# Optimization experiments

Hardware: AMD Instinct MI355X
Metric: run time of the kernel (lower is better)

## Reference

```python
import jax, jax.numpy as jnp
import numpy as np
import math

DIM = 1024
NUM_HEADS = 16


def setup_inputs() -> dict:
    key = jax.random.key(0)
    ks = jax.random.split(key, 6)
    B, S, D = 2, 2048, DIM
    return {
        "q": jax.random.normal(ks[0], (B, S, D), dtype=jnp.float32),
        "k": jax.random.normal(ks[1], (B, S, D), dtype=jnp.float32),
        "v": jax.random.normal(ks[2], (B, S, D), dtype=jnp.float32),
        "wq": jax.random.normal(ks[3], (D, D), dtype=jnp.float32),
        "wk": jax.random.normal(ks[4], (D, D), dtype=jnp.float32),
        "wv": jax.random.normal(ks[5], (D, D), dtype=jnp.float32),
    }


def reference(q, k, v, wq, wk, wv):
    B, S, D = q.shape
    H = NUM_HEADS
    hd = D // H
    # projections: [B,S,D] @ [D,D]
    qp = (q @ wq).reshape(B, H, S, hd)  # NOTE: direct reshape, as in the original
    kp = (k @ wk).reshape(B, H, S, hd)
    vp = (v @ wv).reshape(B, H, S, hd)
    scale = 1.0 / math.sqrt(D)  # original scales by sqrt(dim), not sqrt(head_dim)
    att = jnp.einsum("bhqd,bhkd->bhqk", qp, kp) * scale  # [B,H,S,S]
    att = jax.nn.softmax(att, axis=-1)
    out = jnp.einsum("bhqk,bhkd->bhqd", att, vp)  # [B,H,S,hd]
    out = out.transpose(0, 2, 1, 3).reshape(B, S, D)
    return out
```

## Files before the change

### kernel.cpp

```cpp
#include <hip/hip_runtime.h>
#include <hip/hip_bf16.h>
#include <stdint.h>

#define DIMD 1024
#define SEQ  2048
#define NH   16
#define MROWS 4096
#define NQ   65536

typedef __bf16 bf16_t;
typedef bf16_t bf16x8 __attribute__((ext_vector_type(8)));
typedef float  f32x4  __attribute__((ext_vector_type(4)));
typedef unsigned short u16;
typedef unsigned short u16x4 __attribute__((ext_vector_type(4)));
typedef unsigned short u16x8 __attribute__((ext_vector_type(8)));
typedef unsigned int   u32;
typedef u32 u32x2 __attribute__((ext_vector_type(2)));

static __device__ __forceinline__ f32x4 mfma16(bf16x8 a, bf16x8 b, f32x4 c) {
    return __builtin_amdgcn_mfma_f32_16x16x32_bf16(a, b, c, 0, 0, 0);
}

static __device__ __forceinline__ float fast_exp2(float x) {
#if __has_builtin(__builtin_amdgcn_exp2f)
    return __builtin_amdgcn_exp2f(x);
#else
    return exp2f(x);
#endif
}

#define GLD16(gsrc, ldst) __builtin_amdgcn_global_load_lds(                    \
    (const __attribute__((address_space(1))) unsigned int*)(gsrc),             \
    (__attribute__((address_space(3))) unsigned int*)(ldst), 16, 0, 0)

static __device__ __forceinline__ void split_bf16(float x, u16& h, u16& l) {
    u32 u = __float_as_uint(x);
    u16 hu = (u16)(u >> 16);
    float xh = __uint_as_float((u32)hu << 16);
    float lo = x - xh;
    h = hu;
    l = (u16)(__float_as_uint(lo) >> 16);
}

static __device__ __forceinline__ u32 pack_bf16(float a, float b) {
    return (__float_as_uint(a) >> 16) | (__float_as_uint(b) & 0xffff0000u);
}
static __device__ __forceinline__ u32 pack_bf16_rn(float a, float b) {
    u32 ua = __float_as_uint(a) + 0x8000u;
    u32 ub = __float_as_uint(b) + 0x8000u;
    return (ua >> 16) | (ub & 0xffff0000u);
}
static __device__ __forceinline__ float bf_to_f(u16 v) {
    return __uint_as_float((u32)v << 16);
}

__global__ __launch_bounds__(256) void transWs3(
    const float* __restrict__ w0, const float* __restrict__ w1, const float* __restrict__ w2,
    u16* __restrict__ WTsH, u16* __restrict__ WTsL) {
    const int z = blockIdx.z;
    const float* W = z == 0 ? w0 : z == 1 ? w1 : w2;
    __shared__ u16 Hs[4096], Ls[4096];
    const int tid = threadIdx.x;
    const int kt = blockIdx.x, nt = blockIdx.y;
    const int n0 = nt * 128, k0 = kt * 32;
    #pragma unroll
    for (int i = 0; i < 4; i++) {
        int f = i * 256 + tid;
        int kr = f >> 5, nc4 = (f & 31) * 4;
        f32x4 w = *(const f32x4*)&W[(size_t)(k0 + kr) * DIMD + n0 + nc4];
        int cc = kr >> 3, e = kr & 7;
        #pragma unroll
        for (int j = 0; j < 4; j++) {
            u16 hh, ll; split_bf16(w[j], hh, ll);
            Hs[cc * 1024 + (nc4 + j) * 8 + e] = hh;
            Ls[cc * 1024 + (nc4 + j) * 8 + e] = ll;
        }
    }
    __syncthreads();
    const size_t base = (size_t)z * (DIMD * DIMD) + (size_t)(nt * 32 + kt) * 4096;
    #pragma unroll
    for (int i = 0; i < 2; i++) {
        int idx = (i * 256 + tid) * 8;
        *(u16x8*)(WTsH + base + idx) = *(const u16x8*)&Hs[idx];
        *(u16x8*)(WTsL + base + idx) = *(const u16x8*)&Ls[idx];
    }
}

__global__ __launch_bounds__(256, 3) void proj7(
    const float* __restrict__ xq, const float* __restrict__ xk, const float* __restrict__ xv,
    const u16* __restrict__ WTsH, const u16* __restrict__ WTsL,
    u16* __restrict__ qh, u16* __restrict__ ql,
    u16* __restrict__ kh, u16* __restrict__ kl,
    u16* __restrict__ vh) {

    const int z = blockIdx.z;
    const float* X = z == 0 ? xq : z == 1 ? xk : xv;
    const u16* BH = WTsH + (size_t)z * (DIMD * DIMD);
    const u16* BL = WTsL + (size_t)z * (DIMD * DIMD);
    u16* outH = z == 0 ? qh : z == 1 ? kh : vh;
    u16* outL = z == 0 ? ql : kl;
    const float oscale = z == 0 ? 0.0450842200278f : 1.0f;

    __shared__ u16 lds[24576];
    u16* AsH = lds;
    u16* AsL = lds + 4096;

    const int tid  = threadIdx.x;
    const int lane = tid & 63, wave = tid >> 6;
    const int quad = lane >> 4, l16 = lane & 15;
    const int wy = wave >> 1, wx = wave & 1;
    const int m0 = blockIdx.x * 128;
    const int n0 = blockIdx.y * 128;
    const size_t Bregion0 = (size_t)(blockIdx.y * 32) * 4096;

    const int rA  = tid >> 2, ccA = tid & 3;
    const int idxA0 = ccA * 1024 + ((rA ^ (ccA << 1)) * 8);
    const int idxA1 = idxA0 + 512;
    const float* Xb0 = X + (size_t)(m0 + rA) * DIMD + ccA * 8;
    const float* Xb1 = X + (size_t)(m0 + rA + 64) * DIMD + ccA * 8;

    f32x4 acc[4][4];
    #pragma unroll
    for (int mt = 0; mt < 4; mt++)
        #pragma unroll
        for (int nt = 0; nt < 4; nt++) acc[mt][nt] = (f32x4)0.0f;

    f32x4 pa0, pa1, pa2, pa3;

#define LOADA(kt) do {                                                         \
        pa0 = *(const f32x4*)(Xb0 + (kt) * 32);                                \
        pa1 = *(const f32x4*)(Xb0 + (kt) * 32 + 4);                            \
        pa2 = *(const f32x4*)(Xb1 + (kt) * 32);                                \
        pa3 = *(const f32x4*)(Xb1 + (kt) * 32 + 4);                            \
    } while (0)

#define WRITEA() do {                                                          \
        u16x8 h, l;                                                            \
        _Pragma("unroll")                                                      \
        for (int j = 0; j < 4; j++) {                                          \
            u16 hh, ll;                                                        \
            split_bf16(pa0[j], hh, ll); h[j] = hh;     l[j] = ll;              \
            split_bf16(pa1[j], hh, ll); h[4 + j] = hh; l[4 + j] = ll;          \
        }                                                                      \
        *(u16x8*)&AsH[idxA0] = h;                                              \
        *(u16x8*)&AsL[idxA0] = l;                                              \
        _Pragma("unroll")                                                      \
        for (int j = 0; j < 4; j++) {                                          \
            u16 hh, ll;                                                        \
            split_bf16(pa2[j], hh, ll); h[j] = hh;     l[j] = ll;              \
            split_bf16(pa3[j], hh, ll); h[4 + j] = hh; l[4 + j] = ll;          \
        }                                                                      \
        *(u16x8*)&AsH[idxA1] = h;                                              \
        *(u16x8*)&AsL[idxA1] = l;                                              \
    } while (0)

#define STAGEB(kt, buf) do {                                                   \
        const size_t rb = Bregion0 + (size_t)(kt) * 4096;                      \
        u16* BsHd = lds + 8192 + (buf) * 8192;                                 \
        u16* BsLd = BsHd + 4096;                                               \
        int c0 = tid, c1 = 256 + tid;                                          \
        GLD16(BH + rb + c0 * 8, &BsHd[c0 * 8]);                                \
        GLD16(BH + rb + c1 * 8, &BsHd[c1 * 8]);                                \
        GLD16(BL + rb + c0 * 8, &BsLd[c0 * 8]);                                \
        GLD16(BL + rb + c1 * 8, &BsLd[c1 * 8]);                                \
    } while (0)

    LOADA(0);
    STAGEB(0, 0);
    WRITEA();
    __syncthreads();

    for (int kt = 0; kt < 32; kt++) {
        const int cur = kt & 1;
        if (kt < 31) {
            LOADA(kt + 1);
            STAGEB(kt + 1, cur ^ 1);
        }

        const u16* BsH = lds + 8192 + cur * 8192;
        const u16* BsL = BsH + 4096;

        bf16x8 aH[4], aL[4], bH[4], bL[4];
        #pragma unroll
        for (int mt = 0; mt < 4; mt++) {
            int r = wy * 64 + mt * 16 + l16;
            int idx = quad * 1024 + ((r ^ (quad << 1)) * 8);
            aH[mt] = *(const bf16x8*)&AsH[idx];
            aL[mt] = *(const bf16x8*)&AsL[idx];
        }
        #pragma unroll
        for (int nt = 0; nt < 4; nt++) {
            int r = wx * 64 + nt * 16 + l16;
            bH[nt] = *(const bf16x8*)&BsH[(quad * 128 + r) * 8];
            bL[nt] = *(const bf16x8*)&BsL[(quad * 128 + r) * 8];
        }
        #pragma unroll
        for (int mt = 0; mt < 4; mt++)
            #pragma unroll
            for (int nt = 0; nt < 4; nt++) {
                acc[mt][nt] = mfma16(aH[mt], bH[nt], acc[mt][nt]);
                acc[mt][nt] = mfma16(aH[mt], bL[nt], acc[mt][nt]);
                acc[mt][nt] = mfma16(aL[mt], bH[nt], acc[mt][nt]);
            }

        __syncthreads();
        if (kt < 31) WRITEA();
        __syncthreads();
    }
#undef LOADA
#undef WRITEA
#undef STAGEB

    #pragma unroll
    for (int mt = 0; mt < 4; mt++)
        #pragma unroll
        for (int nt = 0; nt < 4; nt++)
            #pragma unroll
            for (int r = 0; r < 4; r++) {
                int row = m0 + wy * 64 + mt * 16 + quad * 4 + r;
                int col = n0 + wx * 64 + nt * 16 + l16;
                u16 hh, ll; split_bf16(acc[mt][nt][r] * oscale, hh, ll);
                outH[(size_t)row * DIMD + col] = hh;
                if (z != 2) outL[(size_t)row * DIMD + col] = ll;
            }
}

__global__ __launch_bounds__(256) void transposeV(
    const u16* __restrict__ vh, u16* __restrict__ vt) {
    __shared__ u16 Ls[64][72];
    const int tid = threadIdx.x;
    const int bh = blockIdx.y;
    const int s0 = blockIdx.x * 64;
    const size_t slab = (size_t)bh * (SEQ * 64);
    #pragma unroll
    for (int i = 0; i < 2; i++) {
        int f = i * 256 + tid;
        int r = f >> 3, c = (f & 7) * 8;
        *(u16x8*)&Ls[r][c] = *(const u16x8*)(vh + slab + (size_t)(s0 + r) * 64 + c);
    }
    __syncthreads();
    #pragma unroll
    for (int i = 0; i < 2; i++) {
        int f = i * 256 + tid;
        int d = f >> 3, j = (f & 7) * 8;
        u16x8 o;
        #pragma unroll
        for (int jj = 0; jj < 8; jj++) o[jj] = Ls[j + jj][d];
        *(u16x8*)(vt + slab + (size_t)d * SEQ + s0 + j) = o;
    }
}

__global__ __launch_bounds__(256, 2) void flash9(
    const u16* __restrict__ qh, const u16* __restrict__ ql,
    const u16* __restrict__ kh, const u16* __restrict__ kl,
    const u16* __restrict__ vt,
    u16* __restrict__ Opart, float* __restrict__ Mpart, float* __restrict__ Lpart) {

    __shared__ u16 KH[64][72], KL[64][72], VTs[64][72];
    __shared__ u16 Ps[4][16][72];

    const int tid  = threadIdx.x;
    const int lane = tid & 63, wv = tid >> 6;
    const int quad = lane >> 4, l16 = lane & 15;
    const int bh = blockIdx.x, z = blockIdx.z;
    const size_t slab = (size_t)bh * (SEQ * 64);
    const int q0 = blockIdx.y * 128 + wv * 32;
    const int jbase = z * 1024;

    bf16x8 qfH[2][2], qfL[2][2];
    #pragma unroll
    for (int mq = 0; mq < 2; mq++) {
        const size_t rb = slab + (size_t)(q0 + mq * 16 + l16) * 64;
        #pragma unroll
        for (int kk = 0; kk < 2; kk++) {
            qfH[mq][kk] = *(const bf16x8*)(qh + rb + kk * 32 + quad * 8);
            qfL[mq][kk] = *(const bf16x8*)(ql + rb + kk * 32 + quad * 8);
        }
    }

    f32x4 O[2][4];
    float M[2] = {-3.0e38f, -3.0e38f}, L[2] = {0.0f, 0.0f};
    #pragma unroll
    for (int mq = 0; mq < 2; mq++)
        #pragma unroll
        for (int nv = 0; nv < 4; nv++) O[mq][nv] = (f32x4)0.0f;

    const int f0 = tid, f1 = 256 + tid;
    const int r0 = f0 >> 3, c0 = (f0 & 7) * 8;
    const int r1 = f1 >> 3, c1 = (f1 & 7) * 8;
    u16x8 s0, s1, s2, s3, s4, s5;

    {
        const int j0 = jbase;
        s0 = *(const u16x8*)(kh + slab + (size_t)(j0 + r0) * 64 + c0);
        s1 = *(const u16x8*)(kh + slab + (size_t)(j0 + r1) * 64 + c1);
        s2 = *(const u16x8*)(kl + slab + (size_t)(j0 + r0) * 64 + c0);
        s3 = *(const u16x8*)(kl + slab + (size_t)(j0 + r1) * 64 + c1);
        s4 = *(const u16x8*)(vt + slab + (size_t)r0 * SEQ + j0 + c0);
        s5 = *(const u16x8*)(vt + slab + (size_t)r1 * SEQ + j0 + c1);
    }
    *(u16x8*)&KH[r0][c0] = s0;  *(u16x8*)&KH[r1][c1] = s1;
    *(u16x8*)&KL[r0][c0] = s2;  *(u16x8*)&KL[r1][c1] = s3;
    *(u16x8*)&VTs[r0][c0] = s4; *(u16x8*)&VTs[r1][c1] = s5;
    __syncthreads();

    for (int t = 0; t < 16; t++) {
        if (t < 15) {
            const int j0 = jbase + (t + 1) * 64;
            s0 = *(const u16x8*)(kh + slab + (size_t)(j0 + r0) * 64 + c0);
            s1 = *(const u16x8*)(kh + slab + (size_t)(j0 + r1) * 64 + c1);
            s2 = *(const u16x8*)(kl + slab + (size_t)(j0 + r0) * 64 + c0);
            s3 = *(const u16x8*)(kl + slab + (size_t)(j0 + r1) * 64 + c1);
            s4 = *(const u16x8*)(vt + slab + (size_t)r0 * SEQ + j0 + c0);
            s5 = *(const u16x8*)(vt + slab + (size_t)r1 * SEQ + j0 + c1);
        }

        f32x4 St[2][4];
        #pragma unroll
        for (int mq = 0; mq < 2; mq++)
            #pragma unroll
            for (int nt = 0; nt < 4; nt++) St[mq][nt] = (f32x4)0.0f;
        __builtin_amdgcn_s_setprio(1);
        #pragma unroll
        for (int nt = 0; nt < 4; nt++) {
            const int rB = nt * 16 + l16;
            #pragma unroll
            for (int kk = 0; kk < 2; kk++) {
                bf16x8 kHf = *(const bf16x8*)&KH[rB][kk * 32 + quad * 8];
                bf16x8 kLf = *(const bf16x8*)&KL[rB][kk * 32 + quad * 8];
                #pragma unroll
                for (int mq = 0; mq < 2; mq++) {
                    St[mq][nt] = mfma16(kHf, qfH[mq][kk], St[mq][nt]);
                    St[mq][nt] = mfma16(kLf, qfH[mq][kk], St[mq][nt]);
                    St[mq][nt] = mfma16(kHf, qfL[mq][kk], St[mq][nt]);
                }
            }
        }
        __builtin_amdgcn_s_setprio(0);

        #pragma unroll
        for (int mq = 0; mq < 2; mq++) {
            float mx = St[mq][0][0];
            #pragma unroll
            for (int nt = 0; nt < 4; nt++)
                #pragma unroll
                for (int r = 0; r < 4; r++) mx = fmaxf(mx, St[mq][nt][r]);
            mx = fmaxf(mx, __shfl_xor(mx, 16));
            mx = fmaxf(mx, __shfl_xor(mx, 32));
            float Mn = M[mq];
            if (__any(mx > Mn)) {
                Mn = fmaxf(Mn, mx);
                float al = fast_exp2(M[mq] - Mn);
                M[mq] = Mn;
                L[mq] *= al;
                #pragma unroll
                for (int nv = 0; nv < 4; nv++) O[mq][nv] *= al;
            }
            float rs = 0.0f;
            #pragma unroll
            for (int nt = 0; nt < 4; nt++)
                #pragma unroll
                for (int r = 0; r < 4; r++) {
                    float p = fast_exp2(St[mq][nt][r] - Mn);
                    St[mq][nt][r] = p;
                    rs += p;
                }
            rs += __shfl_xor(rs, 16);
            rs += __shfl_xor(rs, 32);
            L[mq] += rs;
            #pragma unroll
            for (int nt = 0; nt < 4; nt++) {
                u32x2 d;
                d[0] = pack_bf16(St[mq][nt][0], St[mq][nt][1]);
                d[1] = pack_bf16(St[mq][nt][2], St[mq][nt][3]);
                *(u32x2*)&Ps[wv][l16][nt * 16 + quad * 4] = d;
            }

            __builtin_amdgcn_s_setprio(1);
            #pragma unroll
            for (int kk = 0; kk < 2; kk++) {
                bf16x8 pB = *(const bf16x8*)&Ps[wv][l16][kk * 32 + quad * 8];
                #pragma unroll
                for (int nv = 0; nv < 4; nv++) {
                    bf16x8 vF = *(const bf16x8*)&VTs[nv * 16 + l16][kk * 32 + quad * 8];
                    O[mq][nv] = mfma16(vF, pB, O[mq][nv]);
                }
            }
            __builtin_amdgcn_s_setprio(0);
        }

        __syncthreads();
        if (t < 15) {
            *(u16x8*)&KH[r0][c0] = s0;  *(u16x8*)&KH[r1][c1] = s1;
            *(u16x8*)&KL[r0][c0] = s2;  *(u16x8*)&KL[r1][c1] = s3;
            *(u16x8*)&VTs[r0][c0] = s4; *(u16x8*)&VTs[r1][c1] = s5;
        }
        __syncthreads();
    }

    const int qgb = bh * SEQ + q0;
    #pragma unroll
    for (int mq = 0; mq < 2; mq++) {
        const int qg = qgb + mq * 16 + l16;
        #pragma unroll
        for (int nv = 0; nv < 4; nv++) {
            u32x2 d;
            d[0] = pack_bf16_rn(O[mq][nv][0], O[mq][nv][1]);
            d[1] = pack_bf16_rn(O[mq][nv][2], O[mq][nv][3]);
            *(u32x2*)(Opart + ((size_t)(z * NQ + qg)) * 64 + nv * 16 + quad * 4) = d;
        }
        if (quad == 0) {
            Mpart[z * NQ + qg] = M[mq];
            Lpart[z * NQ + qg] = L[mq];
        }
    }
}

__global__ __launch_bounds__(256) void combineK(
    const u16* __restrict__ Opart, const float* __restrict__ Mpart,
    const float* __restrict__ Lpart, float* __restrict__ out) {
    int idx = blockIdx.x * 256 + threadIdx.x;
    int qg = idx >> 4, c4 = (idx & 15) * 4;
    float M0 = Mpart[qg], M1 = Mpart[NQ + qg];
    float L0 = Lpart[qg], L1 = Lpart[NQ + qg];
    float Ms = fmaxf(M0, M1);
    float w0 = fast_exp2(M0 - Ms), w1 = fast_exp2(M1 - Ms);
    float inv = 1.0f / (w0 * L0 + w1 * L1);
    u16x4 a = *(const u16x4*)&Opart[(size_t)qg * 64 + c4];
    u16x4 b = *(const u16x4*)&Opart[((size_t)NQ + qg) * 64 + c4];
    f32x4 o;
    #pragma unroll
    for (int j = 0; j < 4; j++)
        o[j] = (w0 * bf_to_f(a[j]) + w1 * bf_to_f(b[j])) * inv;
    int bh = qg >> 11, s = qg & 2047;
    int bb = bh >> 4, h = bh & 15;
    *(f32x4*)&out[((size_t)(bb * SEQ + s)) * DIMD + h * 64 + c4] = o;
}

extern "C" void kernel_launch(void* const* d_in, const int* in_sizes, int n_in,
                              void* d_out, int out_size, void* d_ws, size_t ws_size,
                              hipStream_t stream) {
    const float* q  = (const float*)d_in[0];
    const float* k  = (const float*)d_in[1];
    const float* v  = (const float*)d_in[2];
    const float* wq = (const float*)d_in[3];
    const float* wk = (const float*)d_in[4];
    const float* wv = (const float*)d_in[5];
    float* out = (float*)d_out;

    char* ws = (char*)d_ws;
    const size_t MB = 1 << 20;
    u16* qh   = (u16*)(ws + 0 * MB);
    u16* ql   = (u16*)(ws + 8 * MB);
    u16* kh   = (u16*)(ws + 16 * MB);
    u16* kl   = (u16*)(ws + 24 * MB);
    u16* vh   = (u16*)(ws + 32 * MB);
    u16* vt   = (u16*)(ws + 40 * MB);
    u16* WTsH = (u16*)(ws + 48 * MB);
    u16* WTsL = (u16*)(ws + 54 * MB);
    u16*   Opart = (u16*)(ws + 48 * MB);
    float* Mpart = (float*)(ws + 64 * MB);
    float* Lpart = (float*)(ws + 64 * MB + 512 * 1024);

    transWs3<<<dim3(32, 8, 3), 256, 0, stream>>>(wq, wk, wv, WTsH, WTsL);

    proj7<<<dim3(32, 8, 3), 256, 0, stream>>>(
        q, k, v, WTsH, WTsL, qh, ql, kh, kl, vh);

    transposeV<<<dim3(SEQ / 64, 2 * NH), 256, 0, stream>>>(vh, vt);

    flash9<<<dim3(2 * NH, SEQ / 128, 2), 256, 0, stream>>>(
        qh, ql, kh, kl, vt, Opart, Mpart, Lpart);

    combineK<<<dim3(NQ * 16 / 256), 256, 0, stream>>>(Opart, Mpart, Lpart, out);
}
```

Before: 263.8 us.

## Software-pipeline flash attention: overlap next QK^T with current softmax/PV

Restructures the flash-attention loop so the QK^T MFMA block for tile t+1 is issued before the softmax and PV of tile t, using two score register sets and a double-buffered V tile in shared memory. The P tile buffer is widened so both query subtiles are written before a shared PV loop that reuses each V fragment for both. The launch bound drops the minimum of 2 blocks per CU, which lets the compiler use more registers for the extra score accumulators. The aim is to hide softmax latency behind matrix work, at the risk of lower occupancy and more LDS use.

```diff
diff --git a/kernel.cpp b/kernel.cpp
--- a/kernel.cpp
+++ b/kernel.cpp
@@ -250,14 +250,15 @@
     }
 }
 
-__global__ __launch_bounds__(256, 2) void flash9(
+__global__ __launch_bounds__(256) void flash10(
     const u16* __restrict__ qh, const u16* __restrict__ ql,
     const u16* __restrict__ kh, const u16* __restrict__ kl,
     const u16* __restrict__ vt,
     u16* __restrict__ Opart, float* __restrict__ Mpart, float* __restrict__ Lpart) {
 
-    __shared__ u16 KH[64][72], KL[64][72], VTs[64][72];
-    __shared__ u16 Ps[4][16][72];
+    __shared__ u16 KH[64][72], KL[64][72];
+    __shared__ u16 VT2[2][64][72];
+    __shared__ u16 Ps[4][32][72];
 
     const int tid  = threadIdx.x;
     const int lane = tid & 63, wv = tid >> 6;
@@ -285,118 +286,135 @@
         #pragma unroll
         for (int nv = 0; nv < 4; nv++) O[mq][nv] = (f32x4)0.0f;
 
+    f32x4 StA[2][4], StB[2][4];
+
     const int f0 = tid, f1 = 256 + tid;
     const int r0 = f0 >> 3, c0 = (f0 & 7) * 8;
     const int r1 = f1 >> 3, c1 = (f1 & 7) * 8;
     u16x8 s0, s1, s2, s3, s4, s5;
 
-    {
-        const int j0 = jbase;
-        s0 = *(const u16x8*)(kh + slab + (size_t)(j0 + r0) * 64 + c0);
-        s1 = *(const u16x8*)(kh + slab + (size_t)(j0 + r1) * 64 + c1);
-        s2 = *(const u16x8*)(kl + slab + (size_t)(j0 + r0) * 64 + c0);
-        s3 = *(const u16x8*)(kl + slab + (size_t)(j0 + r1) * 64 + c1);
-        s4 = *(const u16x8*)(vt + slab + (size_t)r0 * SEQ + j0 + c0);
-        s5 = *(const u16x8*)(vt + slab + (size_t)r1 * SEQ + j0 + c1);
-    }
-    *(u16x8*)&KH[r0][c0] = s0;  *(u16x8*)&KH[r1][c1] = s1;
-    *(u16x8*)&KL[r0][c0] = s2;  *(u16x8*)&KL[r1][c1] = s3;
-    *(u16x8*)&VTs[r0][c0] = s4; *(u16x8*)&VTs[r1][c1] = s5;
+#define GLB(j) do {                                                            \
+        const int j0 = jbase + (j) * 64;                                       \
+        s0 = *(const u16x8*)(kh + slab + (size_t)(j0 + r0) * 64 + c0);         \
+        s1 = *(const u16x8*)(kh + slab + (size_t)(j0 + r1) * 64 + c1);         \
+        s2 = *(const u16x8*)(kl + slab + (size_t)(j0 + r0) * 64 + c0);         \
+        s3 = *(const u16x8*)(kl + slab + (size_t)(j0 + r1) * 64 + c1);         \
+        s4 = *(const u16x8*)(vt + slab + (size_t)r0 * SEQ + j0 + c0);          \
+        s5 = *(const u16x8*)(vt + slab + (size_t)r1 * SEQ + j0 + c1);          \
+    } while (0)
+
+#define STAGEW(vb) do {                                                        \
+        *(u16x8*)&KH[r0][c0] = s0;       *(u16x8*)&KH[r1][c1] = s1;            \
+        *(u16x8*)&KL[r0][c0] = s2;       *(u16x8*)&KL[r1][c1] = s3;            \
+        *(u16x8*)&VT2[vb][r0][c0] = s4;  *(u16x8*)&VT2[vb][r1][c1] = s5;       \
+    } while (0)
+
+#define QKPH(St_) do {                                                         \
+        _Pragma("unroll")                                                      \
+        for (int mq = 0; mq < 2; mq++)                                         \
+            _Pragma("unroll")                                                  \
+            for (int nt = 0; nt < 4; nt++) St_[mq][nt] = (f32x4)0.0f;          \
+        __builtin_amdgcn_s_setprio(1);                                         \
+        _Pragma("unroll")                                                      \
+        for (int nt = 0; nt < 4; nt++) {                                       \
+            const int rB = nt * 16 + l16;                                      \
+            _Pragma("unroll")                                                  \
+            for (int kk = 0; kk < 2; kk++) {                                   \
+                bf16x8 kHf = *(const bf16x8*)&KH[rB][kk * 32 + quad * 8];      \
+                bf16x8 kLf = *(const bf16x8*)&KL[rB][kk * 32 + quad * 8];      \
+                _Pragma("unroll")                                              \
+                for (int mq = 0; mq < 2; mq++) {                               \
+                    St_[mq][nt] = mfma16(kHf, qfH[mq][kk], St_[mq][nt]);       \
+                    St_[mq][nt] = mfma16(kLf, qfH[mq][kk], St_[mq][nt]);       \
+                    St_[mq][nt] = mfma16(kHf, qfL[mq][kk], St_[mq][nt]);       \
+                }                                                              \
+            }                                                                  \
+        }                                                                      \
+        __builtin_amdgcn_s_setprio(0);                                         \
+    } while (0)
+
+#define SMPV(St_, vb) do {                                                     \
+        _Pragma("unroll")                                                      \
+        for (int mq = 0; mq < 2; mq++) {                                       \
+            float mx = St_[mq][0][0];                                          \
+            _Pragma("unroll")                                                  \
+            for (int nt = 0; nt < 4; nt++)                                     \
+                _Pragma("unroll")                                              \
+                for (int r = 0; r < 4; r++) mx = fmaxf(mx, St_[mq][nt][r]);    \
+            mx = fmaxf(mx, __shfl_xor(mx, 16));                                \
+            mx = fmaxf(mx, __shfl_xor(mx, 32));                                \
+            float Mn = M[mq];                                                  \
+            if (__any(mx > Mn)) {                                              \
+                Mn = fmaxf(Mn, mx);                                            \
+                float al = fast_exp2(M[mq] - Mn);                              \
+                M[mq] = Mn;                                                    \
+                L[mq] *= al;                                                   \
+                _Pragma("unroll")                                              \
+                for (int nv = 0; nv < 4; nv++) O[mq][nv] *= al;                \
+            }                                                                  \
+            float rs = 0.0f;                                                   \
+            _Pragma("unroll")                                                  \
+            for (int nt = 0; nt < 4; nt++)                                     \
+                _Pragma("unroll")                                              \
+                for (int r = 0; r < 4; r++) {                                  \
+                    float p = fast_exp2(St_[mq][nt][r] - Mn);                  \
+                    St_[mq][nt][r] = p;                                        \
+                    rs += p;                                                   \
+                }                                                              \
+            rs += __shfl_xor(rs, 16);                                          \
+            rs += __shfl_xor(rs, 32);                                          \
+            L[mq] += rs;                                                       \
+            _Pragma("unroll")                                                  \
+            for (int nt = 0; nt < 4; nt++) {                                   \
+                u32x2 d;                                                       \
+                d[0] = pack_bf16(St_[mq][nt][0], St_[mq][nt][1]);              \
+                d[1] = pack_bf16(St_[mq][nt][2], St_[mq][nt][3]);              \
+                *(u32x2*)&Ps[wv][mq * 16 + l16][nt * 16 + quad * 4] = d;       \
+            }                                                                  \
+        }                                                                      \
+        __builtin_amdgcn_s_setprio(1);                                         \
+        _Pragma("unroll")                                                      \
+        for (int kk = 0; kk < 2; kk++) {                                       \
+            bf16x8 pB[2];                                                      \
+            _Pragma("unroll")                                                  \
+            for (int mq = 0; mq < 2; mq++)                                     \
+                pB[mq] = *(const bf16x8*)&Ps[wv][mq * 16 + l16][kk * 32 + quad * 8]; \
+            _Pragma("unroll")                                                  \
+            for (int nv = 0; nv < 4; nv++) {                                   \
+                bf16x8 vF = *(const bf16x8*)&VT2[vb][nv * 16 + l16][kk * 32 + quad * 8]; \
+                _Pragma("unroll")                                              \
+                for (int mq = 0; mq < 2; mq++)                                 \
+                    O[mq][nv] = mfma16(vF, pB[mq], O[mq][nv]);                 \
+            }                                                                  \
+        }                                                                      \
+        __builtin_amdgcn_s_setprio(0);                                         \
+    } while (0)
+
+    GLB(0);
+    STAGEW(0);
+    GLB(1);
     __syncthreads();
-
-    for (int t = 0; t < 16; t++) {
-        if (t < 15) {
-            const int j0 = jbase + (t + 1) * 64;
-            s0 = *(const u16x8*)(kh + slab + (size_t)(j0 + r0) * 64 + c0);
-            s1 = *(const u16x8*)(kh + slab + (size_t)(j0 + r1) * 64 + c1);
-            s2 = *(const u16x8*)(kl + slab + (size_t)(j0 + r0) * 64 + c0);
-            s3 = *(const u16x8*)(kl + slab + (size_t)(j0 + r1) * 64 + c1);
-            s4 = *(const u16x8*)(vt + slab + (size_t)r0 * SEQ + j0 + c0);
-            s5 = *(const u16x8*)(vt + slab + (size_t)r1 * SEQ + j0 + c1);
-        }
-
-        f32x4 St[2][4];
-        #pragma unroll
-        for (int mq = 0; mq < 2; mq++)
-            #pragma unroll
-            for (int nt = 0; nt < 4; nt++) St[mq][nt] = (f32x4)0.0f;
-        __builtin_amdgcn_s_setprio(1);
-        #pragma unroll
-        for (int nt = 0; nt < 4; nt++) {
-            const int rB = nt * 16 + l16;
-            #pragma unroll
-            for (int kk = 0; kk < 2; kk++) {
-                bf16x8 kHf = *(const bf16x8*)&KH[rB][kk * 32 + quad * 8];
-                bf16x8 kLf = *(const bf16x8*)&KL[rB][kk * 32 + quad * 8];
-                #pragma unroll
-                for (int mq = 0; mq < 2; mq++) {
-                    St[mq][nt] = mfma16(kHf, qfH[mq][kk], St[mq][nt]);
-                    St[mq][nt] = mfma16(kLf, qfH[mq][kk], St[mq][nt]);
-                    St[mq][nt] = mfma16(kHf, qfL[mq][kk], St[mq][nt]);
-                }
-            }
-        }
-        __builtin_amdgcn_s_setprio(0);
-
-        #pragma unroll
-        for (int mq = 0; mq < 2; mq++) {
-            float mx = St[mq][0][0];
-            #pragma unroll
-            for (int nt = 0; nt < 4; nt++)
-                #pragma unroll
-                for (int r = 0; r < 4; r++) mx = fmaxf(mx, St[mq][nt][r]);
-            mx = fmaxf(mx, __shfl_xor(mx, 16));
-            mx = fmaxf(mx, __shfl_xor(mx, 32));
-            float Mn = M[mq];
-            if (__any(mx > Mn)) {
-                Mn = fmaxf(Mn, mx);
-                float al = fast_exp2(M[mq] - Mn);
-                M[mq] = Mn;
-                L[mq] *= al;
-                #pragma unroll
-                for (int nv = 0; nv < 4; nv++) O[mq][nv] *= al;
-            }
-            float rs = 0.0f;
-            #pragma unroll
-            for (int nt = 0; nt < 4; nt++)
-                #pragma unroll
-                for (int r = 0; r < 4; r++) {
-                    float p = fast_exp2(St[mq][nt][r] - Mn);
-                    St[mq][nt][r] = p;
-                    rs += p;
-                }
-            rs += __shfl_xor(rs, 16);
-            rs += __shfl_xor(rs, 32);
-            L[mq] += rs;
-            #pragma unroll
-            for (int nt = 0; nt < 4; nt++) {
-                u32x2 d;
-                d[0] = pack_bf16(St[mq][nt][0], St[mq][nt][1]);
-                d[1] = pack_bf16(St[mq][nt][2], St[mq][nt][3]);
-                *(u32x2*)&Ps[wv][l16][nt * 16 + quad * 4] = d;
-            }
-
-            __builtin_amdgcn_s_setprio(1);
-            #pragma unroll
-            for (int kk = 0; kk < 2; kk++) {
-                bf16x8 pB = *(const bf16x8*)&Ps[wv][l16][kk * 32 + quad * 8];
-                #pragma unroll
-                for (int nv = 0; nv < 4; nv++) {
-                    bf16x8 vF = *(const bf16x8*)&VTs[nv * 16 + l16][kk * 32 + quad * 8];
-                    O[mq][nv] = mfma16(vF, pB, O[mq][nv]);
-                }
-            }
-            __builtin_amdgcn_s_setprio(0);
-        }
-
-        __syncthreads();
-        if (t < 15) {
-            *(u16x8*)&KH[r0][c0] = s0;  *(u16x8*)&KH[r1][c1] = s1;
-            *(u16x8*)&KL[r0][c0] = s2;  *(u16x8*)&KL[r1][c1] = s3;
-            *(u16x8*)&VTs[r0][c0] = s4; *(u16x8*)&VTs[r1][c1] = s5;
-        }
-        __syncthreads();
-    }
+    QKPH(StA);
+    __syncthreads();
+
+    for (int t = 0; t < 16; t += 2) {
+        if (t + 1 < 16) STAGEW(1);
+        if (t + 2 < 16) GLB(t + 2);
+        __syncthreads();
+        if (t + 1 < 16) QKPH(StB);
+        SMPV(StA, 0);
+        __syncthreads();
+        if (t + 2 < 16) STAGEW(0);
+        if (t + 3 < 16) GLB(t + 3);
+        __syncthreads();
+        if (t + 2 < 16) QKPH(StA);
+        SMPV(StB, 1);
+        __syncthreads();
+    }
+#undef GLB
+#undef STAGEW
+#undef QKPH
+#undef SMPV
 
     const int qgb = bh * SEQ + q0;
     #pragma unroll
@@ -469,7 +487,7 @@
 
     transposeV<<<dim3(SEQ / 64, 2 * NH), 256, 0, stream>>>(vh, vt);
 
-    flash9<<<dim3(2 * NH, SEQ / 128, 2), 256, 0, stream>>>(
+    flash10<<<dim3(2 * NH, SEQ / 128, 2), 256, 0, stream>>>(
         qh, ql, kh, kl, vt, Opart, Mpart, Lpart);
 
     combineK<<<dim3(NQ * 16 / 256), 256, 0, stream>>>(Opart, Mpart, Lpart, out);
```

After: 317.2 us. 1.2x slower.
